# Kernel optimization log

Measured on AMD Instinct MI355X. Metric: run time of the kernel, lower is better.

## Reference

```python
import jax, jax.numpy as jnp
from jax import lax
import numpy as np

# Heaviside spike with surrogate gradient (sdyt ~ d/dx tanh(x)); fwd is exact.
@jax.custom_vjp
def spike(x):
    return (x > 0).astype(x.dtype)

def _spike_fwd(x):
    return (x > 0).astype(x.dtype), x

def _spike_bwd(x, g):
    t = jnp.tanh(x)
    return (g * (1.0 - t * t),)

spike.defvjp(_spike_fwd, _spike_bwd)

def dyt(x, alpha, gamma, beta):
    # Dynamic Tanh norm: gamma * tanh(alpha * x) + beta
    return gamma * jnp.tanh(alpha * x) + beta

def slstm_seq(x, Wih, Whh, bih, bhh, thr, c0, h0):
    """Sequential SLSTM (snntorch, reset_mechanism='none') over a full sequence.
    x: [B,S,D]; Wih:[4H,D]; Whh:[4H,H]. Returns spikes [B,S,H], final (c, h)."""
    xg = jnp.einsum('bsd,gd->bsg', x, Wih) + bih  # precompute input gates [B,S,4H]

    def step(carry, xg_t):
        c, h = carry
        g = xg_t + h @ Whh.T + bhh
        i, f, gg, o = jnp.split(g, 4, axis=-1)  # torch LSTMCell gate order
        c = jax.nn.sigmoid(f) * c + jax.nn.sigmoid(i) * jnp.tanh(gg)
        h = jax.nn.sigmoid(o) * jnp.tanh(c)
        spk = spike(h - thr)
        return (c, h), spk

    (c, h), spks = lax.scan(step, (c0, h0), jnp.swapaxes(xg, 0, 1))
    return jnp.swapaxes(spks, 0, 1), c, h


def setup_inputs() -> dict:
    key = jax.random.key(0)
    ks = jax.random.split(key, 16)
    B, S, H, V, L = 4, 256, 512, 32000, 2
    G = 4 * H
    sc = 0.02
    d = {}
    d['src'] = jax.random.randint(ks[0], (B, S), 0, V)
    d['tgt'] = jax.random.randint(ks[1], (B, S), 0, V)
    d['emb_enc'] = jax.random.normal(ks[2], (V, H), jnp.float32) * sc
    d['enc_norm_alpha'] = jnp.full((1,), 0.5, jnp.float32)
    d['enc_norm_gamma'] = jnp.ones((H,), jnp.float32)
    d['enc_norm_beta'] = jnp.zeros((H,), jnp.float32)
    d['enc_Wih'] = jax.random.normal(ks[3], (L, G, H), jnp.float32) * sc
    d['enc_Whh'] = jax.random.normal(ks[4], (L, G, H), jnp.float32) * sc
    d['enc_bih'] = jnp.zeros((L, G), jnp.float32)
    d['enc_bhh'] = jnp.zeros((L, G), jnp.float32)
    d['enc_thr'] = jnp.ones((L, H), jnp.float32)
    d['emb_dec'] = jax.random.normal(ks[5], (V, H), jnp.float32) * sc
    d['dec_norm_alpha'] = jnp.full((1,), 0.5, jnp.float32)
    d['dec_norm_gamma'] = jnp.ones((H,), jnp.float32)
    d['dec_norm_beta'] = jnp.zeros((H,), jnp.float32)
    d['dec_Wih'] = jax.random.normal(ks[6], (L, G, H), jnp.float32) * sc
    d['dec_Whh'] = jax.random.normal(ks[7], (L, G, H), jnp.float32) * sc
    d['dec_bih'] = jnp.zeros((L, G), jnp.float32)
    d['dec_bhh'] = jnp.zeros((L, G), jnp.float32)
    d['dec_thr'] = jnp.ones((L, H), jnp.float32)
    d['dec_fc_W'] = jax.random.normal(ks[8], (L, H, H), jnp.float32) * sc
    d['dec_fc_b'] = jnp.zeros((L, H), jnp.float32)
    d['dec_dyt_alpha'] = jnp.full((L,), 0.5, jnp.float32)
    d['dec_dyt_gamma'] = jnp.ones((L, H), jnp.float32)
    d['dec_dyt_beta'] = jnp.zeros((L, H), jnp.float32)
    d['out_W'] = jax.random.normal(ks[9], (V, H), jnp.float32) * sc
    d['out_b'] = jnp.zeros((V,), jnp.float32)
    return d


def reference(src, tgt, emb_enc, enc_norm_alpha, enc_norm_gamma, enc_norm_beta,
              enc_Wih, enc_Whh, enc_bih, enc_bhh, enc_thr,
              emb_dec, dec_norm_alpha, dec_norm_gamma, dec_norm_beta,
              dec_Wih, dec_Whh, dec_bih, dec_bhh, dec_thr,
              dec_fc_W, dec_fc_b, dec_dyt_alpha, dec_dyt_gamma, dec_dyt_beta,
              out_W, out_b):
    L, _, H = enc_Wih.shape[0], enc_Wih.shape[1], enc_Wih.shape[2]
    B = src.shape[0]
    PAD = 0
    c0 = jnp.zeros((B, H), emb_enc.dtype)
    h0 = jnp.zeros((B, H), emb_enc.dtype)

    # ---- Encoder (note: non-bidirectional path feeds `src` to every layer, as in source) ----
    e_enc = emb_enc.at[PAD].set(0.0)  # padding_idx row is zero
    src_e = dyt(e_enc[src], enc_norm_alpha, enc_norm_gamma, enc_norm_beta)  # [B,S,H]
    syns, mems = [], []
    for l in range(L):
        _, c, h = slstm_seq(src_e, enc_Wih[l], enc_Whh[l], enc_bih[l], enc_bhh[l],
                            enc_thr[l], c0, h0)
        syns.append(c)
        mems.append(h)

    # ---- Decoder ----
    e_dec = emb_dec.at[PAD].set(0.0)
    x = dyt(e_dec[tgt], dec_norm_alpha, dec_norm_gamma, dec_norm_beta)  # [B,S,H]
    for l in range(L):
        spks, _, _ = slstm_seq(x, dec_Wih[l], dec_Whh[l], dec_bih[l], dec_bhh[l],
                               dec_thr[l], syns[l], mems[l])
        y = jnp.einsum('bsh,oh->bso', spks, dec_fc_W[l]) + dec_fc_b[l]
        if l > 0:  # residual=i>0
            y = y + x
        x = dyt(y, dec_dyt_alpha[l], dec_dyt_gamma[l], dec_dyt_beta[l])

    return jnp.einsum('bsh,vh->bsv', x, out_W) + out_b  # [B,S,V] logits
```

## Files before the change

kernel.cpp:

```cpp
#include <hip/hip_runtime.h>
#include <cstddef>

#define S_LEN 256
#define H_DIM 512

typedef __attribute__((ext_vector_type(8))) short bf16x8;
typedef __attribute__((ext_vector_type(4))) float f32x4;
typedef __attribute__((ext_vector_type(8))) unsigned short u16x8;

__device__ __forceinline__ float sigf(float x) { return 1.0f / (1.0f + expf(-x)); }

__device__ __forceinline__ unsigned short cvt_bf16(float f) {
  unsigned u = __float_as_uint(f);
  u += 0x7fffu + ((u >> 16) & 1u);
  return (unsigned short)(u >> 16);
}
__device__ __forceinline__ float bf2f(unsigned short s) {
  return __uint_as_float(((unsigned)s) << 16);
}

__global__ void zero_kernel(float* __restrict__ p, int n4) {
  int i = blockIdx.x * blockDim.x + threadIdx.x;
  if (i < n4) ((float4*)p)[i] = make_float4(0.f, 0.f, 0.f, 0.f);
}

__global__ __launch_bounds__(256)
void cvt_f32_bf16(const float* __restrict__ in, unsigned short* __restrict__ out,
                  int n4) {
  int i = blockIdx.x * blockDim.x + threadIdx.x;
  if (i < n4) {
    float4 v = ((const float4*)in)[i];
    ushort4 r;
    r.x = cvt_bf16(v.x); r.y = cvt_bf16(v.y);
    r.z = cvt_bf16(v.z); r.w = cvt_bf16(v.w);
    ((ushort4*)out)[i] = r;
  }
}

__global__ __launch_bounds__(128)
void embed_dyt(const int* __restrict__ idx, const float* __restrict__ E,
               const float* __restrict__ alpha_p, const float* __restrict__ gamma,
               const float* __restrict__ beta, unsigned short* __restrict__ out) {
  const int row = blockIdx.x;
  const int t4  = threadIdx.x * 4;
  const int id  = idx[row];
  const float al = alpha_p[0];
  float4 e = make_float4(0.f, 0.f, 0.f, 0.f);
  if (id != 0) e = *(const float4*)(E + (size_t)id * H_DIM + t4);
  const float4 g = *(const float4*)(gamma + t4);
  const float4 b = *(const float4*)(beta + t4);
  ushort4 o;
  o.x = cvt_bf16(g.x * tanhf(al * e.x) + b.x);
  o.y = cvt_bf16(g.y * tanhf(al * e.y) + b.y);
  o.z = cvt_bf16(g.z * tanhf(al * e.z) + b.z);
  o.w = cvt_bf16(g.w * tanhf(al * e.w) + b.w);
  *(ushort4*)(out + (size_t)row * H_DIM + t4) = o;
}

__global__ __launch_bounds__(256)
void gemm_bt_bf16(const unsigned short* __restrict__ A,
                  const float* __restrict__ Bf,
                  const float* __restrict__ bias,
                  float* __restrict__ C, int N, int K) {
  __shared__ unsigned short As[128 * 64];
  __shared__ unsigned short Bs[128 * 64];
  const int tid = threadIdx.x;
  const int bm = blockIdx.x * 128, bn = blockIdx.y * 128;
  const int lane = tid & 63;
  const int wr = (tid >> 7) & 1, wc = (tid >> 6) & 1;
  f32x4 acc[4][4] = {};

  const int srow = tid >> 3;
  const int ss   = tid & 7;

  for (int k0 = 0; k0 < K; k0 += 64) {
    __syncthreads();
#pragma unroll
    for (int p = 0; p < 4; ++p) {
      const int row = srow + p * 32;
      const int ps = ss ^ (row & 7);
      u16x8 va = *(const u16x8*)(A + (size_t)(bm + row) * K + k0 + ss * 8);
      *(u16x8*)(As + row * 64 + ps * 8) = va;
      const float* bp = Bf + (size_t)(bn + row) * K + k0 + ss * 8;
      const float4 b0 = *(const float4*)(bp);
      const float4 b1 = *(const float4*)(bp + 4);
      u16x8 vb;
      vb[0] = cvt_bf16(b0.x); vb[1] = cvt_bf16(b0.y);
      vb[2] = cvt_bf16(b0.z); vb[3] = cvt_bf16(b0.w);
      vb[4] = cvt_bf16(b1.x); vb[5] = cvt_bf16(b1.y);
      vb[6] = cvt_bf16(b1.z); vb[7] = cvt_bf16(b1.w);
      *(u16x8*)(Bs + row * 64 + ps * 8) = vb;
    }
    __syncthreads();
#pragma unroll
    for (int ks = 0; ks < 2; ++ks) {
      const int r16 = lane & 15;
      const int kslot = ks * 4 + (lane >> 4);
      bf16x8 af[4], bfr[4];
#pragma unroll
      for (int m = 0; m < 4; ++m) {
        const int row = wr * 64 + m * 16 + r16;
        af[m] = *(const bf16x8*)(As + row * 64 + (kslot ^ (row & 7)) * 8);
      }
#pragma unroll
      for (int n = 0; n < 4; ++n) {
        const int row = wc * 64 + n * 16 + r16;
        bfr[n] = *(const bf16x8*)(Bs + row * 64 + (kslot ^ (row & 7)) * 8);
      }
#pragma unroll
      for (int m = 0; m < 4; ++m)
#pragma unroll
        for (int n = 0; n < 4; ++n)
          acc[m][n] = __builtin_amdgcn_mfma_f32_16x16x32_bf16(af[m], bfr[n],
                                                              acc[m][n], 0, 0, 0);
    }
  }

  const int r16 = lane & 15, rg = lane >> 4;
#pragma unroll
  for (int m = 0; m < 4; ++m) {
#pragma unroll
    for (int n = 0; n < 4; ++n) {
      const int col = bn + wc * 64 + n * 16 + r16;
      const float bb = bias[col];
      const int rowb = bm + wr * 64 + m * 16 + rg * 4;
#pragma unroll
      for (int r = 0; r < 4; ++r)
        C[(size_t)(rowb + r) * N + col] = acc[m][n][r] + bb;
    }
  }
}

__device__ __forceinline__ void rec_core(
    int g, int t, int tid,
    const float* __restrict__ xg, int xg_stride,
    const unsigned short* __restrict__ Whh, const float* __restrict__ bhh,
    const float* __restrict__ h_in, float* __restrict__ h_out,
    float* __restrict__ c,
    float* __restrict__ spk, const float* __restrict__ thr,
    float* __restrict__ hs, float (*__restrict__ gred)[4]) {
  const int lr = tid >> 3, kc = tid & 7;
  const int q = lr >> 3, ci = lr & 7;
  const int c0 = g * 8;
  const int grow = q * H_DIM + c0 + ci;
  float xgv[4] = {0.f, 0.f, 0.f, 0.f};
  if (kc == 0) {
#pragma unroll
    for (int b = 0; b < 4; ++b)
      xgv[b] = xg[(size_t)(b * S_LEN + t) * xg_stride + grow];
  }
  {
    const float4* s4 = (const float4*)h_in;
    float4* d4 = (float4*)hs;
    d4[tid] = s4[tid];
    d4[tid + 256] = s4[tid + 256];
  }
  __syncthreads();
  const unsigned short* wrow = Whh + (size_t)grow * H_DIM;
  float acc[4] = {0.f, 0.f, 0.f, 0.f};
#pragma unroll
  for (int it = 0; it < 8; ++it) {
    const int k = it * 64 + kc * 8;
    const u16x8 wv = *(const u16x8*)(wrow + k);
    const float w0 = bf2f(wv[0]), w1 = bf2f(wv[1]), w2 = bf2f(wv[2]), w3 = bf2f(wv[3]);
    const float w4 = bf2f(wv[4]), w5 = bf2f(wv[5]), w6 = bf2f(wv[6]), w7 = bf2f(wv[7]);
#pragma unroll
    for (int b = 0; b < 4; ++b) {
      const float4 hA = *(const float4*)&hs[b * H_DIM + k];
      const float4 hB = *(const float4*)&hs[b * H_DIM + k + 4];
      acc[b] += w0 * hA.x + w1 * hA.y + w2 * hA.z + w3 * hA.w
              + w4 * hB.x + w5 * hB.y + w6 * hB.z + w7 * hB.w;
    }
  }
#pragma unroll
  for (int off = 1; off < 8; off <<= 1) {
#pragma unroll
    for (int b = 0; b < 4; ++b) acc[b] += __shfl_xor(acc[b], off);
  }
  if (kc == 0) {
    const float bb = bhh[grow];
#pragma unroll
    for (int b = 0; b < 4; ++b) gred[lr][b] = acc[b] + xgv[b] + bb;
  }
  __syncthreads();
  if (tid < 32) {
    const int b = tid & 3, cc = tid >> 2;
    const int col = c0 + cc;
    const float gi = gred[cc][b];
    const float gf = gred[8 + cc][b];
    const float gg = gred[16 + cc][b];
    const float go = gred[24 + cc][b];
    const float cold = c[b * H_DIM + col];
    const float cn = sigf(gf) * cold + sigf(gi) * tanhf(gg);
    const float hn = sigf(go) * tanhf(cn);
    c[b * H_DIM + col] = cn;
    h_out[b * H_DIM + col] = hn;
    if (spk)
      spk[(size_t)(b * S_LEN + t) * H_DIM + col] = (hn - thr[col]) > 0.f ? 1.f : 0.f;
  }
}

struct StepInst {
  const float* xg;
  const unsigned short* Whh;
  const float* bhh;
  float* c;
  const float* h_in;
  float* h_out;
  int xg_stride;
};

__global__ __launch_bounds__(256)
void slstm_step(StepInst I0, StepInst I1, int t) {
  __shared__ float hs[4 * H_DIM];
  __shared__ float gred[32][4];
  StepInst I = (blockIdx.x < 64) ? I0 : I1;
  rec_core(blockIdx.x & 63, t, threadIdx.x, I.xg, I.xg_stride, I.Whh, I.bhh,
           I.h_in, I.h_out, I.c, nullptr, nullptr, hs, gred);
}

struct DecArgs {
  const float* xg0;
  float*       xg1;
  const unsigned short* Whh0bf; const unsigned short* Whh1bf;
  const float* bhh0; const float* bhh1;
  const unsigned short* Wih1bf; const float* bih1;
  const float* fc0W; const float* fc0b;
  const float* fc1W; const float* fc1b;
  const float* dyt_a;
  const float* dyt_g;
  const float* dyt_b;
  const float* thr0; const float* thr1;
  float* c0; float* c1;
  const float* h0_init; const float* h1_init;
  float* ring0; float* ring1;
  float* spk0; float* spk1;
  float* x1;
  unsigned short* x2;
};

__device__ __forceinline__ void stage_rows(const float* __restrict__ src, int t,
                                           int tid, float* hs) {
  float4* d4 = (float4*)hs;
  const int f0 = tid, f1 = tid + 256;
  d4[f0] = *(const float4*)(src + (size_t)((f0 >> 7) * S_LEN + t) * H_DIM + (f0 & 127) * 4);
  d4[f1] = *(const float4*)(src + (size_t)((f1 >> 7) * S_LEN + t) * H_DIM + (f1 & 127) * 4);
}

__global__ __launch_bounds__(256)
void dec_slot(DecArgs A, int s) {
  __shared__ float hs[4 * H_DIM];
  __shared__ float gred[32][4];
  const int bid = blockIdx.x;
  const int tid = threadIdx.x;

  if (bid < 64) {
    const int t = s;
    if (t < 256) {
      const float* h_in = (t == 0) ? A.h0_init : (A.ring0 + (size_t)(t & 1) * 2048);
      float* h_out = A.ring0 + (size_t)((t + 1) & 1) * 2048;
      rec_core(bid, t, tid, A.xg0, 2048, A.Whh0bf, A.bhh0, h_in, h_out, A.c0,
               A.spk0, A.thr0, hs, gred);
    }
  } else if (bid < 128) {
    const int t = s - 3;
    if (t >= 0 && t < 256) {
      const float* h_in = (t == 0) ? A.h1_init : (A.ring1 + (size_t)(t & 1) * 2048);
      float* h_out = A.ring1 + (size_t)((t + 1) & 1) * 2048;
      rec_core(bid - 64, t, tid, A.xg1, 2048, A.Whh1bf, A.bhh1, h_in, h_out, A.c1,
               A.spk1, A.thr1, hs, gred);
    }
  } else if (bid < 192) {
    const int t = s - 2;
    if (t >= 0 && t < 256) {
      stage_rows(A.x1, t, tid, hs);
      __syncthreads();
      const int wc = bid - 128;
      const int lr = tid >> 3, kc = tid & 7;
      const int row = wc * 32 + lr;
      const unsigned short* wrow = A.Wih1bf + (size_t)row * H_DIM;
      float acc[4] = {0.f, 0.f, 0.f, 0.f};
#pragma unroll
      for (int it = 0; it < 8; ++it) {
        const int k = it * 64 + kc * 8;
        const u16x8 wv = *(const u16x8*)(wrow + k);
        const float w0 = bf2f(wv[0]), w1 = bf2f(wv[1]), w2 = bf2f(wv[2]), w3 = bf2f(wv[3]);
        const float w4 = bf2f(wv[4]), w5 = bf2f(wv[5]), w6 = bf2f(wv[6]), w7 = bf2f(wv[7]);
#pragma unroll
        for (int b = 0; b < 4; ++b) {
          const float4 hA = *(const float4*)&hs[b * H_DIM + k];
          const float4 hB = *(const float4*)&hs[b * H_DIM + k + 4];
          acc[b] += w0 * hA.x + w1 * hA.y + w2 * hA.z + w3 * hA.w
                  + w4 * hB.x + w5 * hB.y + w6 * hB.z + w7 * hB.w;
        }
      }
#pragma unroll
      for (int off = 1; off < 8; off <<= 1) {
#pragma unroll
        for (int b = 0; b < 4; ++b) acc[b] += __shfl_xor(acc[b], off);
      }
      if (kc == 0) {
        const float bb = A.bih1[row];
#pragma unroll
        for (int b = 0; b < 4; ++b)
          A.xg1[(size_t)(b * S_LEN + t) * 2048 + row] = acc[b] + bb;
      }
    }
  } else {
    const bool isB = (bid < 224);
    const int t = isB ? (s - 1) : (s - 4);
    if (t >= 0 && t < 256) {
      const float* spk = isB ? A.spk0 : A.spk1;
      const float* fcW = isB ? A.fc0W : A.fc1W;
      const float* fcb = isB ? A.fc0b : A.fc1b;
      const int lidx = isB ? 0 : 1;
      stage_rows(spk, t, tid, hs);
      __syncthreads();
      const int wb = bid - (isB ? 192 : 224);
      const int lr = tid >> 4, kc = tid & 15;
      const int col = wb * 16 + lr;
      const float* wrow = fcW + (size_t)col * H_DIM;
      float a0 = 0.f, a1 = 0.f, a2 = 0.f, a3 = 0.f;
#pragma unroll
      for (int it = 0; it < 8; ++it) {
        const int k = kc * 32 + it * 4;
        const float4 w  = *(const float4*)(wrow + k);
        const float4 h0 = *(const float4*)&hs[0 * H_DIM + k];
        const float4 h1 = *(const float4*)&hs[1 * H_DIM + k];
        const float4 h2 = *(const float4*)&hs[2 * H_DIM + k];
        const float4 h3 = *(const float4*)&hs[3 * H_DIM + k];
        a0 += w.x * h0.x + w.y * h0.y + w.z * h0.z + w.w * h0.w;
        a1 += w.x * h1.x + w.y * h1.y + w.z * h1.z + w.w * h1.w;
        a2 += w.x * h2.x + w.y * h2.y + w.z * h2.z + w.w * h2.w;
        a3 += w.x * h3.x + w.y * h3.y + w.z * h3.z + w.w * h3.w;
      }
#pragma unroll
      for (int off = 1; off < 16; off <<= 1) {
        a0 += __shfl_xor(a0, off);
        a1 += __shfl_xor(a1, off);
        a2 += __shfl_xor(a2, off);
        a3 += __shfl_xor(a3, off);
      }
      if (kc == 0) {
        const float al = A.dyt_a[lidx];
        const float gm = A.dyt_g[lidx * H_DIM + col];
        const float be = A.dyt_b[lidx * H_DIM + col];
        const float bb = fcb[col];
        float v[4] = {a0, a1, a2, a3};
#pragma unroll
        for (int b = 0; b < 4; ++b) {
          float y = v[b] + bb;
          if (!isB) y += A.x1[(size_t)(b * S_LEN + t) * H_DIM + col];
          const float r = gm * tanhf(al * y) + be;
          if (isB) A.x1[(size_t)(b * S_LEN + t) * H_DIM + col] = r;
          else     A.x2[(size_t)(b * S_LEN + t) * H_DIM + col] = cvt_bf16(r);
        }
      }
    }
  }
}

extern "C" void kernel_launch(void* const* d_in, const int* in_sizes, int n_in,
                              void* d_out, int out_size, void* d_ws, size_t ws_size,
                              hipStream_t stream) {
  (void)in_sizes; (void)n_in; (void)out_size; (void)ws_size;
  const int*   src       = (const int*)d_in[0];
  const int*   tgt       = (const int*)d_in[1];
  const float* emb_enc   = (const float*)d_in[2];
  const float* enc_alpha = (const float*)d_in[3];
  const float* enc_gamma = (const float*)d_in[4];
  const float* enc_beta  = (const float*)d_in[5];
  const float* enc_Wih   = (const float*)d_in[6];
  const float* enc_Whh   = (const float*)d_in[7];
  const float* enc_bih   = (const float*)d_in[8];
  const float* enc_bhh   = (const float*)d_in[9];
  const float* emb_dec   = (const float*)d_in[11];
  const float* dec_alpha = (const float*)d_in[12];
  const float* dec_gamma = (const float*)d_in[13];
  const float* dec_beta  = (const float*)d_in[14];
  const float* dec_Wih   = (const float*)d_in[15];
  const float* dec_Whh   = (const float*)d_in[16];
  const float* dec_bih   = (const float*)d_in[17];
  const float* dec_bhh   = (const float*)d_in[18];
  const float* dec_thr   = (const float*)d_in[19];
  const float* dec_fc_W  = (const float*)d_in[20];
  const float* dec_fc_b  = (const float*)d_in[21];
  const float* dyt_alpha = (const float*)d_in[22];
  const float* dyt_gamma = (const float*)d_in[23];
  const float* dyt_beta  = (const float*)d_in[24];
  const float* out_W     = (const float*)d_in[25];
  const float* out_b     = (const float*)d_in[26];
  float* out = (float*)d_out;

  float* ws = (float*)d_ws;
  float*          x1        = ws;
  float*          xg_enc    = ws + 524288;
  float*          xg_d0     = xg_enc;
  float*          xg_d1     = xg_enc + 2097152;
  float*          spk0      = ws + 4718592;
  float*          spk1      = ws + 5242880;
  unsigned short* src_e_bf  = (unsigned short*)(ws + 5767168);
  unsigned short* dec_x0_bf = (unsigned short*)(ws + 5898240);
  unsigned short* x2_bf     = (unsigned short*)(ws + 6029312);
  unsigned short* wbf       = (unsigned short*)(ws + 6160384);
  float* st = ws + 7660544;
  float* zbuf    = st;
  float* c0buf   = st + 2048;
  float* c1buf   = st + 4096;
  float* ring_e0 = st + 6144;
  float* ring_e1 = st + 10240;
  float* ring_d0 = st + 14336;
  float* ring_d1 = st + 18432;

  zero_kernel<<<6, 256, 0, stream>>>(st, 1536);
  embed_dyt<<<1024, 128, 0, stream>>>(src, emb_enc, enc_alpha, enc_gamma, enc_beta,
                                      src_e_bf);
  embed_dyt<<<1024, 128, 0, stream>>>(tgt, emb_dec, dec_alpha, dec_gamma, dec_beta,
                                      dec_x0_bf);

  cvt_f32_bf16<<<2048, 256, 0, stream>>>(enc_Whh, wbf, 524288);

  gemm_bt_bf16<<<dim3(8, 32), 256, 0, stream>>>(src_e_bf, enc_Wih, enc_bih,
                                                xg_enc, 4096, 512);

  for (int t = 0; t < 256; ++t) {
    StepInst A, B;
    A.xg = xg_enc;        A.Whh = wbf;                A.bhh = enc_bhh;
    A.c = c0buf;
    A.h_in  = (t == 0) ? zbuf : ring_e0 + (t & 1) * 2048;
    A.h_out = ring_e0 + ((t + 1) & 1) * 2048;
    A.xg_stride = 4096;
    B.xg = xg_enc + 2048; B.Whh = wbf + 1048576;      B.bhh = enc_bhh + 2048;
    B.c = c1buf;
    B.h_in  = (t == 0) ? zbuf : ring_e1 + (t & 1) * 2048;
    B.h_out = ring_e1 + ((t + 1) & 1) * 2048;
    B.xg_stride = 4096;
    slstm_step<<<128, 256, 0, stream>>>(A, B, t);
  }

  cvt_f32_bf16<<<2048, 256, 0, stream>>>(dec_Whh, wbf, 524288);
  cvt_f32_bf16<<<1024, 256, 0, stream>>>(dec_Wih + 1048576, wbf + 2097152, 262144);

  gemm_bt_bf16<<<dim3(8, 16), 256, 0, stream>>>(dec_x0_bf, dec_Wih, dec_bih,
                                                xg_d0, 2048, 512);

  DecArgs D;
  D.xg0 = xg_d0;              D.xg1 = xg_d1;
  D.Whh0bf = wbf;             D.Whh1bf = wbf + 1048576;
  D.bhh0 = dec_bhh;           D.bhh1 = dec_bhh + 2048;
  D.Wih1bf = wbf + 2097152;   D.bih1 = dec_bih + 2048;
  D.fc0W = dec_fc_W;          D.fc0b = dec_fc_b;
  D.fc1W = dec_fc_W + 262144; D.fc1b = dec_fc_b + 512;
  D.dyt_a = dyt_alpha;        D.dyt_g = dyt_gamma;     D.dyt_b = dyt_beta;
  D.thr0 = dec_thr;           D.thr1 = dec_thr + 512;
  D.c0 = c0buf;               D.c1 = c1buf;
  D.h0_init = ring_e0;        D.h1_init = ring_e1;
  D.ring0 = ring_d0;          D.ring1 = ring_d1;
  D.spk0 = spk0;              D.spk1 = spk1;
  D.x1 = x1;                  D.x2 = x2_bf;

  for (int s = 0; s < 260; ++s)
    dec_slot<<<256, 256, 0, stream>>>(D, s);

  gemm_bt_bf16<<<dim3(8, 250), 256, 0, stream>>>(x2_bf, out_W, out_b,
                                                 out, 32000, 512);
}
```

Measured before the change: 2.575 ms.

## Fuse decoder layer-1 input projection into its recurrent step, shorten pipeline

```diff
diff --git a/kernel.cpp b/kernel.cpp
--- a/kernel.cpp
+++ b/kernel.cpp
@@ -38,17 +38,26 @@
 }
 
 __global__ __launch_bounds__(128)
-void embed_dyt(const int* __restrict__ idx, const float* __restrict__ E,
-               const float* __restrict__ alpha_p, const float* __restrict__ gamma,
-               const float* __restrict__ beta, unsigned short* __restrict__ out) {
-  const int row = blockIdx.x;
-  const int t4  = threadIdx.x * 4;
-  const int id  = idx[row];
-  const float al = alpha_p[0];
+void embed_dyt2(const int* __restrict__ idxA, const float* __restrict__ EA,
+                const float* __restrict__ alA, const float* __restrict__ gmA,
+                const float* __restrict__ btA, unsigned short* __restrict__ outA,
+                const int* __restrict__ idxB, const float* __restrict__ EB,
+                const float* __restrict__ alB, const float* __restrict__ gmB,
+                const float* __restrict__ btB, unsigned short* __restrict__ outB) {
+  const bool isA = blockIdx.x < 1024;
+  const int row = isA ? blockIdx.x : (blockIdx.x - 1024);
+  const int* idx = isA ? idxA : idxB;
+  const float* E = isA ? EA : EB;
+  const float al = (isA ? alA : alB)[0];
+  const float* gm = isA ? gmA : gmB;
+  const float* bt = isA ? btA : btB;
+  unsigned short* out = isA ? outA : outB;
+  const int t4 = threadIdx.x * 4;
+  const int id = idx[row];
   float4 e = make_float4(0.f, 0.f, 0.f, 0.f);
   if (id != 0) e = *(const float4*)(E + (size_t)id * H_DIM + t4);
-  const float4 g = *(const float4*)(gamma + t4);
-  const float4 b = *(const float4*)(beta + t4);
+  const float4 g = *(const float4*)(gm + t4);
+  const float4 b = *(const float4*)(bt + t4);
   ushort4 o;
   o.x = cvt_bf16(g.x * tanhf(al * e.x) + b.x);
   o.y = cvt_bf16(g.y * tanhf(al * e.y) + b.y);
@@ -221,10 +230,9 @@
 
 struct DecArgs {
   const float* xg0;
-  float*       xg1;
   const unsigned short* Whh0bf; const unsigned short* Whh1bf;
   const float* bhh0; const float* bhh1;
-  const unsigned short* Wih1bf; const float* bih1;
+  const float* Wih1; const float* bih1;
   const float* fc0W; const float* fc0b;
   const float* fc1W; const float* fc1b;
   const float* dyt_a;
@@ -240,8 +248,8 @@
 };
 
 __device__ __forceinline__ void stage_rows(const float* __restrict__ src, int t,
-                                           int tid, float* hs) {
-  float4* d4 = (float4*)hs;
+                                           int tid, float* dst) {
+  float4* d4 = (float4*)dst;
   const int f0 = tid, f1 = tid + 256;
   d4[f0] = *(const float4*)(src + (size_t)((f0 >> 7) * S_LEN + t) * H_DIM + (f0 & 127) * 4);
   d4[f1] = *(const float4*)(src + (size_t)((f1 >> 7) * S_LEN + t) * H_DIM + (f1 & 127) * 4);
@@ -250,6 +258,7 @@
 __global__ __launch_bounds__(256)
 void dec_slot(DecArgs A, int s) {
   __shared__ float hs[4 * H_DIM];
+  __shared__ float xs[4 * H_DIM];
   __shared__ float gred[32][4];
   const int bid = blockIdx.x;
   const int tid = threadIdx.x;
@@ -263,52 +272,84 @@
                A.spk0, A.thr0, hs, gred);
     }
   } else if (bid < 128) {
-    const int t = s - 3;
+    const int t = s - 2;
     if (t >= 0 && t < 256) {
+      const int g = bid - 64;
       const float* h_in = (t == 0) ? A.h1_init : (A.ring1 + (size_t)(t & 1) * 2048);
       float* h_out = A.ring1 + (size_t)((t + 1) & 1) * 2048;
-      rec_core(bid - 64, t, tid, A.xg1, 2048, A.Whh1bf, A.bhh1, h_in, h_out, A.c1,
-               A.spk1, A.thr1, hs, gred);
-    }
-  } else if (bid < 192) {
-    const int t = s - 2;
-    if (t >= 0 && t < 256) {
-      stage_rows(A.x1, t, tid, hs);
+      {
+        const float4* s4 = (const float4*)h_in;
+        float4* d4 = (float4*)hs;
+        d4[tid] = s4[tid];
+        d4[tid + 256] = s4[tid + 256];
+        stage_rows(A.x1, t, tid, xs);
+      }
       __syncthreads();
-      const int wc = bid - 128;
       const int lr = tid >> 3, kc = tid & 7;
-      const int row = wc * 32 + lr;
-      const unsigned short* wrow = A.Wih1bf + (size_t)row * H_DIM;
+      const int q = lr >> 3, ci = lr & 7;
+      const int c0 = g * 8;
+      const int grow = q * H_DIM + c0 + ci;
       float acc[4] = {0.f, 0.f, 0.f, 0.f};
-#pragma unroll
-      for (int it = 0; it < 8; ++it) {
-        const int k = it * 64 + kc * 8;
-        const u16x8 wv = *(const u16x8*)(wrow + k);
-        const float w0 = bf2f(wv[0]), w1 = bf2f(wv[1]), w2 = bf2f(wv[2]), w3 = bf2f(wv[3]);
-        const float w4 = bf2f(wv[4]), w5 = bf2f(wv[5]), w6 = bf2f(wv[6]), w7 = bf2f(wv[7]);
-#pragma unroll
-        for (int b = 0; b < 4; ++b) {
-          const float4 hA = *(const float4*)&hs[b * H_DIM + k];
-          const float4 hB = *(const float4*)&hs[b * H_DIM + k + 4];
-          acc[b] += w0 * hA.x + w1 * hA.y + w2 * hA.z + w3 * hA.w
-                  + w4 * hB.x + w5 * hB.y + w6 * hB.z + w7 * hB.w;
+      {
+        const unsigned short* wrow = A.Whh1bf + (size_t)grow * H_DIM;
+#pragma unroll
+        for (int it = 0; it < 8; ++it) {
+          const int k = it * 64 + kc * 8;
+          const u16x8 wv = *(const u16x8*)(wrow + k);
+          const float w0 = bf2f(wv[0]), w1 = bf2f(wv[1]), w2 = bf2f(wv[2]), w3 = bf2f(wv[3]);
+          const float w4 = bf2f(wv[4]), w5 = bf2f(wv[5]), w6 = bf2f(wv[6]), w7 = bf2f(wv[7]);
+#pragma unroll
+          for (int b = 0; b < 4; ++b) {
+            const float4 hA = *(const float4*)&hs[b * H_DIM + k];
+            const float4 hB = *(const float4*)&hs[b * H_DIM + k + 4];
+            acc[b] += w0 * hA.x + w1 * hA.y + w2 * hA.z + w3 * hA.w
+                    + w4 * hB.x + w5 * hB.y + w6 * hB.z + w7 * hB.w;
+          }
         }
       }
+      {
+        const float* vrow = A.Wih1 + (size_t)grow * H_DIM;
+#pragma unroll
+        for (int it = 0; it < 16; ++it) {
+          const int k = it * 32 + kc * 4;
+          const float4 w = *(const float4*)(vrow + k);
+#pragma unroll
+          for (int b = 0; b < 4; ++b) {
+            const float4 xv = *(const float4*)&xs[b * H_DIM + k];
+            acc[b] += w.x * xv.x + w.y * xv.y + w.z * xv.z + w.w * xv.w;
+          }
+        }
+      }
 #pragma unroll
       for (int off = 1; off < 8; off <<= 1) {
 #pragma unroll
         for (int b = 0; b < 4; ++b) acc[b] += __shfl_xor(acc[b], off);
       }
       if (kc == 0) {
-        const float bb = A.bih1[row];
-#pragma unroll
-        for (int b = 0; b < 4; ++b)
-          A.xg1[(size_t)(b * S_LEN + t) * 2048 + row] = acc[b] + bb;
+        const float bb = A.bhh1[grow] + A.bih1[grow];
+#pragma unroll
+        for (int b = 0; b < 4; ++b) gred[lr][b] = acc[b] + bb;
+      }
+      __syncthreads();
+      if (tid < 32) {
+        const int b = tid & 3, cc = tid >> 2;
+        const int col = c0 + cc;
+        const float gi = gred[cc][b];
+        const float gf = gred[8 + cc][b];
+        const float gg = gred[16 + cc][b];
+        const float go = gred[24 + cc][b];
+        const float cold = A.c1[b * H_DIM + col];
+        const float cn = sigf(gf) * cold + sigf(gi) * tanhf(gg);
+        const float hn = sigf(go) * tanhf(cn);
+        A.c1[b * H_DIM + col] = cn;
+        h_out[b * H_DIM + col] = hn;
+        A.spk1[(size_t)(b * S_LEN + t) * H_DIM + col] =
+            (hn - A.thr1[col]) > 0.f ? 1.f : 0.f;
       }
     }
   } else {
-    const bool isB = (bid < 224);
-    const int t = isB ? (s - 1) : (s - 4);
+    const bool isB = (bid < 160);
+    const int t = isB ? (s - 1) : (s - 3);
     if (t >= 0 && t < 256) {
       const float* spk = isB ? A.spk0 : A.spk1;
       const float* fcW = isB ? A.fc0W : A.fc1W;
@@ -316,7 +357,7 @@
       const int lidx = isB ? 0 : 1;
       stage_rows(spk, t, tid, hs);
       __syncthreads();
-      const int wb = bid - (isB ? 192 : 224);
+      const int wb = bid - (isB ? 128 : 160);
       const int lr = tid >> 4, kc = tid & 15;
       const int col = wb * 16 + lr;
       const float* wrow = fcW + (size_t)col * H_DIM;
@@ -396,14 +437,14 @@
   float*          x1        = ws;
   float*          xg_enc    = ws + 524288;
   float*          xg_d0     = xg_enc;
-  float*          xg_d1     = xg_enc + 2097152;
   float*          spk0      = ws + 4718592;
   float*          spk1      = ws + 5242880;
   unsigned short* src_e_bf  = (unsigned short*)(ws + 5767168);
-  unsigned short* dec_x0_bf = (unsigned short*)(ws + 5898240);
-  unsigned short* x2_bf     = (unsigned short*)(ws + 6029312);
-  unsigned short* wbf       = (unsigned short*)(ws + 6160384);
-  float* st = ws + 7660544;
+  unsigned short* dec_x0_bf = (unsigned short*)(ws + 6029312);
+  unsigned short* x2_bf     = (unsigned short*)(ws + 6291456);
+  unsigned short* wbf_enc   = (unsigned short*)(ws + 6553600);
+  unsigned short* wbf_dec   = (unsigned short*)(ws + 7602176);
+  float* st = ws + 8650752;
   float* zbuf    = st;
   float* c0buf   = st + 2048;
   float* c1buf   = st + 4096;
@@ -413,24 +454,24 @@
   float* ring_d1 = st + 18432;
 
   zero_kernel<<<6, 256, 0, stream>>>(st, 1536);
-  embed_dyt<<<1024, 128, 0, stream>>>(src, emb_enc, enc_alpha, enc_gamma, enc_beta,
-                                      src_e_bf);
-  embed_dyt<<<1024, 128, 0, stream>>>(tgt, emb_dec, dec_alpha, dec_gamma, dec_beta,
-                                      dec_x0_bf);
-
-  cvt_f32_bf16<<<2048, 256, 0, stream>>>(enc_Whh, wbf, 524288);
+  cvt_f32_bf16<<<2048, 256, 0, stream>>>(enc_Whh, wbf_enc, 524288);
+  cvt_f32_bf16<<<2048, 256, 0, stream>>>(dec_Whh, wbf_dec, 524288);
+  embed_dyt2<<<2048, 128, 0, stream>>>(src, emb_enc, enc_alpha, enc_gamma, enc_beta,
+                                       src_e_bf,
+                                       tgt, emb_dec, dec_alpha, dec_gamma, dec_beta,
+                                       dec_x0_bf);
 
   gemm_bt_bf16<<<dim3(8, 32), 256, 0, stream>>>(src_e_bf, enc_Wih, enc_bih,
                                                 xg_enc, 4096, 512);
 
   for (int t = 0; t < 256; ++t) {
     StepInst A, B;
-    A.xg = xg_enc;        A.Whh = wbf;                A.bhh = enc_bhh;
+    A.xg = xg_enc;        A.Whh = wbf_enc;             A.bhh = enc_bhh;
     A.c = c0buf;
     A.h_in  = (t == 0) ? zbuf : ring_e0 + (t & 1) * 2048;
     A.h_out = ring_e0 + ((t + 1) & 1) * 2048;
     A.xg_stride = 4096;
-    B.xg = xg_enc + 2048; B.Whh = wbf + 1048576;      B.bhh = enc_bhh + 2048;
+    B.xg = xg_enc + 2048; B.Whh = wbf_enc + 1048576;   B.bhh = enc_bhh + 2048;
     B.c = c1buf;
     B.h_in  = (t == 0) ? zbuf : ring_e1 + (t & 1) * 2048;
     B.h_out = ring_e1 + ((t + 1) & 1) * 2048;
@@ -438,17 +479,14 @@
     slstm_step<<<128, 256, 0, stream>>>(A, B, t);
   }
 
-  cvt_f32_bf16<<<2048, 256, 0, stream>>>(dec_Whh, wbf, 524288);
-  cvt_f32_bf16<<<1024, 256, 0, stream>>>(dec_Wih + 1048576, wbf + 2097152, 262144);
-
   gemm_bt_bf16<<<dim3(8, 16), 256, 0, stream>>>(dec_x0_bf, dec_Wih, dec_bih,
                                                 xg_d0, 2048, 512);
 
   DecArgs D;
-  D.xg0 = xg_d0;              D.xg1 = xg_d1;
-  D.Whh0bf = wbf;             D.Whh1bf = wbf + 1048576;
+  D.xg0 = xg_d0;
+  D.Whh0bf = wbf_dec;         D.Whh1bf = wbf_dec + 1048576;
   D.bhh0 = dec_bhh;           D.bhh1 = dec_bhh + 2048;
-  D.Wih1bf = wbf + 2097152;   D.bih1 = dec_bih + 2048;
+  D.Wih1 = dec_Wih + 1048576; D.bih1 = dec_bih + 2048;
   D.fc0W = dec_fc_W;          D.fc0b = dec_fc_b;
   D.fc1W = dec_fc_W + 262144; D.fc1b = dec_fc_b + 512;
   D.dyt_a = dyt_alpha;        D.dyt_g = dyt_gamma;     D.dyt_b = dyt_beta;
@@ -459,8 +497,8 @@
   D.spk0 = spk0;              D.spk1 = spk1;
   D.x1 = x1;                  D.x2 = x2_bf;
 
-  for (int s = 0; s < 260; ++s)
-    dec_slot<<<256, 256, 0, stream>>>(D, s);
+  for (int s = 0; s < 259; ++s)
+    dec_slot<<<192, 256, 0, stream>>>(D, s);
 
   gemm_bt_bf16<<<dim3(8, 250), 256, 0, stream>>>(x2_bf, out_W, out_b,
                                                  out, 32000, 512);
```

Measured after the change: 2.670 ms. 3.7% more time.
